# Optimization experiments

Hardware: AMD Instinct MI355X
Metric: run time of the kernel (lower is better)

Reference implementation:

```python
import jax, jax.numpy as jnp
import numpy as np

B, S, DEC, ENC = 64, 4096, 512, 256


def setup_inputs() -> dict:
    key = jax.random.key(0)
    ks = jax.random.split(key, 8)
    scale_d = 1.0 / np.sqrt(DEC)
    scale_e = 1.0 / np.sqrt(ENC)
    return {
        "decoder_hidden": jax.random.normal(ks[0], (B, 1, DEC), jnp.float32),
        "encoder_outputs": jax.random.normal(ks[1], (B, S, ENC), jnp.float32),
        "mask": jax.random.randint(ks[2], (B, S), 0, 2, jnp.int32),
        "Wd": jax.random.normal(ks[3], (DEC, ENC), jnp.float32) * scale_d,
        "bd": jnp.zeros((ENC,), jnp.float32),
        "We": jax.random.normal(ks[4], (ENC, ENC), jnp.float32) * scale_e,
        "be": jnp.zeros((ENC,), jnp.float32),
        "Wa": jax.random.normal(ks[5], (ENC,), jnp.float32) * scale_e,
        "ba": jnp.zeros((1,), jnp.float32),
    }


def reference(decoder_hidden, encoder_outputs, mask, Wd, bd, We, be, Wa, ba):
    # decoder_proj: [B,1,ENC]; encoder_proj: [B,S,ENC]
    decoder_proj = jnp.einsum("bqd,de->bqe", decoder_hidden, Wd) + bd
    encoder_proj = jnp.einsum("bse,ef->bsf", encoder_outputs, We) + be
    energy = jnp.tanh(decoder_proj + encoder_proj)          # [B,S,ENC]
    scores = jnp.einsum("bse,e->bs", energy, Wa) + ba[0]     # [B,S]
    scores = jnp.where(mask == 0, jnp.float32(-1e10), scores)
    attn = jax.nn.softmax(scores, axis=1)                    # [B,S]
    context = jnp.einsum("bs,bse->be", attn, encoder_outputs)[:, None, :]  # [B,1,ENC]
    return context, attn
```

## Files before the change

### kernel.cpp

```cpp
#include <hip/hip_runtime.h>

#define BATCH 64
#define SEQ   4096
#define DECD  512
#define ENC   256
#define TS    64
#define NCHUNK (SEQ / TS)
#define OUT_ATTN (BATCH * ENC)

typedef short  short8  __attribute__((ext_vector_type(8)));
typedef float  floatx4 __attribute__((ext_vector_type(4)));

__device__ __forceinline__ short f2bf(float f) {
    union { float f; unsigned u; } v; v.f = f;
    unsigned u = v.u;
    u += 0x7FFFu + ((u >> 16) & 1u);
    return (short)(u >> 16);
}

__device__ __forceinline__ float fast_tanh(float x) {
    x = fminf(fmaxf(x, -9.0f), 9.0f);
    float e2 = __expf(2.0f * x);
    float r  = __builtin_amdgcn_rcpf(e2 + 1.0f);
    return fmaf(-2.0f, r, 1.0f);
}

__device__ __forceinline__ void gload_lds16(const short* g, short* l) {
    __builtin_amdgcn_global_load_lds(
        (const __attribute__((address_space(1))) unsigned int*)g,
        (__attribute__((address_space(3))) unsigned int*)l,
        16, 0, 0);
}

__global__ void dp_kernel(const float* __restrict__ dh,
                          const float* __restrict__ Wd,
                          const float* __restrict__ bd,
                          const float* __restrict__ be,
                          float* __restrict__ dpb) {
    __shared__ float dhs[DECD];
    int b = blockIdx.x, t = threadIdx.x;
    dhs[t]       = dh[b * DECD + t];
    dhs[t + 256] = dh[b * DECD + t + 256];
    __syncthreads();
    float a0 = 0.f, a1 = 0.f, a2 = 0.f, a3 = 0.f;
#pragma unroll 4
    for (int d = 0; d < DECD; d += 4) {
        a0 = fmaf(dhs[d],     Wd[(d)     * ENC + t], a0);
        a1 = fmaf(dhs[d + 1], Wd[(d + 1) * ENC + t], a1);
        a2 = fmaf(dhs[d + 2], Wd[(d + 2) * ENC + t], a2);
        a3 = fmaf(dhs[d + 3], Wd[(d + 3) * ENC + t], a3);
    }
    dpb[b * ENC + t] = bd[t] + be[t] + ((a0 + a1) + (a2 + a3));
}

__global__ void pack_kernel(const float* __restrict__ We, short* __restrict__ WeF) {
    int gid  = blockIdx.x * 256 + threadIdx.x;
    int lane = gid & 63;
    int nt   = (gid >> 6) & 15;
    int kt   = gid >> 10;
    int quad = lane >> 4, l16 = lane & 15;
    int n = nt * 16 + l16;
    short8 v;
#pragma unroll
    for (int j = 0; j < 8; ++j) {
        int k = kt * 32 + quad * 8 + j;
        v[j] = f2bf(We[k * ENC + n]);
    }
    *(short8*)(WeF + gid * 8) = v;
}

__global__ __launch_bounds__(256, 4) void main_kernel(
    const float* __restrict__ enc, const int* __restrict__ mask,
    const short* __restrict__ WeF, const float* __restrict__ dpb,
    const float* __restrict__ Wa, const float* __restrict__ ba,
    float* __restrict__ out, float* __restrict__ ctx_ws, float* __restrict__ ml_ws)
{
    __shared__ short bsl[2][8192];
    __shared__ float sc[TS];
    __shared__ float dpbs[ENC];
    __shared__ float was[ENC];

    int blk   = blockIdx.x;
    int b     = blk >> 6;
    int chunk = blk & 63;
    int s_base = chunk * TS;
    int t    = threadIdx.x;
    int w    = t >> 6, lane = t & 63;
    int quad = lane >> 4, l16 = lane & 15;

    const float* encB = enc + (size_t)b * SEQ * ENC;
    int row = s_base + w * 16 + l16;
    const float* aRow = encB + (size_t)row * ENC + quad * 8;

    dpbs[t] = dpb[b * ENC + t];
    was[t]  = Wa[t];

    floatx4 acc[16];
#pragma unroll
    for (int nt = 0; nt < 16; ++nt) acc[nt] = (floatx4){0.f, 0.f, 0.f, 0.f};

#pragma unroll
    for (int j = 0; j < 4; ++j)
        gload_lds16(WeF + j * 2048 + (w * 64 + lane) * 8, &bsl[0][0] + j * 2048 + w * 512);

    floatx4 x0 = *(const floatx4*)(aRow);
    floatx4 x1 = *(const floatx4*)(aRow + 4);

    for (int kt = 0; kt < 8; ++kt) {
        __syncthreads();
        if (kt < 7) {
            const short* g = WeF + (kt + 1) * 8192;
            short* lb = &bsl[(kt + 1) & 1][0];
#pragma unroll
            for (int j = 0; j < 4; ++j)
                gload_lds16(g + j * 2048 + (w * 64 + lane) * 8, lb + j * 2048 + w * 512);
        }
        floatx4 nx0, nx1;
        if (kt < 7) {
            nx0 = *(const floatx4*)(aRow + (kt + 1) * 32);
            nx1 = *(const floatx4*)(aRow + (kt + 1) * 32 + 4);
        }
        short8 a;
#pragma unroll
        for (int j = 0; j < 4; ++j) { a[j] = f2bf(x0[j]); a[j + 4] = f2bf(x1[j]); }
        const short* bp = &bsl[kt & 1][0] + lane * 8;
#pragma unroll
        for (int nt = 0; nt < 16; ++nt) {
            short8 bf = *(const short8*)(bp + nt * 512);
            acc[nt] = __builtin_amdgcn_mfma_f32_16x16x32_bf16(a, bf, acc[nt], 0, 0, 0);
        }
        if (kt < 7) { x0 = nx0; x1 = nx1; }
    }

    float ba0 = ba[0];
    float part[4] = {0.f, 0.f, 0.f, 0.f};
#pragma unroll
    for (int nt = 0; nt < 16; ++nt) {
        int n = nt * 16 + l16;
        float wa  = was[n];
        float dpv = dpbs[n];
#pragma unroll
        for (int r = 0; r < 4; ++r)
            part[r] = fmaf(wa, fast_tanh(acc[nt][r] + dpv), part[r]);
    }
#pragma unroll
    for (int r = 0; r < 4; ++r) {
        float v = part[r];
        v += __shfl_xor(v, 1);
        v += __shfl_xor(v, 2);
        v += __shfl_xor(v, 4);
        v += __shfl_xor(v, 8);
        part[r] = v;
    }
    if (l16 == 0) {
        int idx0 = w * 16 + quad * 4;
        int s0 = s_base + idx0;
        const int4 mv = *(const int4*)(mask + b * SEQ + s0);
        int mvals[4] = {mv.x, mv.y, mv.z, mv.w};
#pragma unroll
        for (int r = 0; r < 4; ++r) {
            float scv = part[r] + ba0;
            if (mvals[r] == 0) scv = -1e10f;
            sc[idx0 + r] = scv;
            out[OUT_ATTN + (size_t)b * SEQ + s0 + r] = scv;
        }
    }
    __syncthreads();

    float v = sc[lane];
    float m = v;
    m = fmaxf(m, __shfl_xor(m, 1));
    m = fmaxf(m, __shfl_xor(m, 2));
    m = fmaxf(m, __shfl_xor(m, 4));
    m = fmaxf(m, __shfl_xor(m, 8));
    m = fmaxf(m, __shfl_xor(m, 16));
    m = fmaxf(m, __shfl_xor(m, 32));
    float e = __expf(v - m);
    float l = e;
    l += __shfl_xor(l, 1);
    l += __shfl_xor(l, 2);
    l += __shfl_xor(l, 4);
    l += __shfl_xor(l, 8);
    l += __shfl_xor(l, 16);
    l += __shfl_xor(l, 32);

    float c0 = 0.f, c1 = 0.f, c2 = 0.f, c3 = 0.f;
    const float* ep = encB + (size_t)s_base * ENC + t;
#pragma unroll 4
    for (int s2 = 0; s2 < TS; s2 += 4) {
        float w0 = __shfl(e, s2);
        float w1 = __shfl(e, s2 + 1);
        float w2 = __shfl(e, s2 + 2);
        float w3 = __shfl(e, s2 + 3);
        c0 = fmaf(w0, ep[(size_t)(s2)     * ENC], c0);
        c1 = fmaf(w1, ep[(size_t)(s2 + 1) * ENC], c1);
        c2 = fmaf(w2, ep[(size_t)(s2 + 2) * ENC], c2);
        c3 = fmaf(w3, ep[(size_t)(s2 + 3) * ENC], c3);
    }
    float ctx = (c0 + c1) + (c2 + c3);

    int cidx = b * NCHUNK + chunk;
    ctx_ws[(size_t)cidx * ENC + t] = ctx;
    if (t == 0) {
        ml_ws[cidx * 2]     = m;
        ml_ws[cidx * 2 + 1] = l;
    }
}

__global__ void final_kernel(const float* __restrict__ ctx_ws,
                             const float* __restrict__ ml_ws,
                             float* __restrict__ out) {
    int b = blockIdx.x, t = threadIdx.x;
    float m = -3.4e38f;
    for (int c = 0; c < NCHUNK; ++c)
        m = fmaxf(m, ml_ws[(b * NCHUNK + c) * 2]);
    float L = 0.f;
    for (int c = 0; c < NCHUNK; ++c)
        L += ml_ws[(b * NCHUNK + c) * 2 + 1] * __expf(ml_ws[(b * NCHUNK + c) * 2] - m);
    float inv = 1.0f / L;

    float cx = 0.f;
    for (int c = 0; c < NCHUNK; ++c)
        cx += ctx_ws[(size_t)(b * NCHUNK + c) * ENC + t] * __expf(ml_ws[(b * NCHUNK + c) * 2] - m);
    out[b * ENC + t] = cx * inv;

    for (int s = t; s < SEQ; s += 256) {
        float raw = out[OUT_ATTN + (size_t)b * SEQ + s];
        out[OUT_ATTN + (size_t)b * SEQ + s] = __expf(raw - m) * inv;
    }
}

extern "C" void kernel_launch(void* const* d_in, const int* in_sizes, int n_in,
                              void* d_out, int out_size, void* d_ws, size_t ws_size,
                              hipStream_t stream) {
    const float* dh   = (const float*)d_in[0];
    const float* enc  = (const float*)d_in[1];
    const int*   mask = (const int*)d_in[2];
    const float* Wd   = (const float*)d_in[3];
    const float* bd   = (const float*)d_in[4];
    const float* We   = (const float*)d_in[5];
    const float* be   = (const float*)d_in[6];
    const float* Wa   = (const float*)d_in[7];
    const float* ba   = (const float*)d_in[8];
    float* out = (float*)d_out;

    float* w      = (float*)d_ws;
    float* ctx_ws = w;
    float* ml_ws  = w + BATCH * NCHUNK * ENC;
    float* dpbuf  = ml_ws + BATCH * NCHUNK * 2;
    short* WeF    = (short*)(dpbuf + BATCH * ENC);

    hipLaunchKernelGGL(dp_kernel,   dim3(BATCH),           dim3(256), 0, stream, dh, Wd, bd, be, dpbuf);
    hipLaunchKernelGGL(pack_kernel, dim3(32),              dim3(256), 0, stream, We, WeF);
    hipLaunchKernelGGL(main_kernel, dim3(BATCH * NCHUNK),  dim3(256), 0, stream,
                       enc, mask, WeF, dpbuf, Wa, ba, out, ctx_ws, ml_ws);
    hipLaunchKernelGGL(final_kernel, dim3(BATCH),          dim3(256), 0, stream, ctx_ws, ml_ws, out);
}
```

Before: 444.1 us.

## Enlarge sequence tile, drop LDS B staging, split dp projection and context reduction

Raises the sequence tile from 64 to 256 rows per block with 512 threads. Each wave now computes two 16-row M tiles so every B fragment feeds two MFMAs, and B is read straight from global/L2 instead of being double-buffered through LDS with barriers. A-operand loads are prefetched three K-steps ahead. The decoder projection is split across 4 blocks per batch and summed in the main kernel, and the context partial sums are split over two thread halves with weights staged in LDS. This trades fewer blocks and more registers for less LDS traffic and fewer barriers, and leaves a redundant dpbs store that is immediately overwritten.

```diff
diff --git a/kernel.cpp b/kernel.cpp
--- a/kernel.cpp
+++ b/kernel.cpp
@@ -4,7 +4,7 @@
 #define SEQ   4096
 #define DECD  512
 #define ENC   256
-#define TS    64
+#define TS    256
 #define NCHUNK (SEQ / TS)
 #define OUT_ATTN (BATCH * ENC)
 
@@ -25,32 +25,28 @@
     return fmaf(-2.0f, r, 1.0f);
 }
 
-__device__ __forceinline__ void gload_lds16(const short* g, short* l) {
-    __builtin_amdgcn_global_load_lds(
-        (const __attribute__((address_space(1))) unsigned int*)g,
-        (__attribute__((address_space(3))) unsigned int*)l,
-        16, 0, 0);
-}
-
 __global__ void dp_kernel(const float* __restrict__ dh,
                           const float* __restrict__ Wd,
                           const float* __restrict__ bd,
                           const float* __restrict__ be,
-                          float* __restrict__ dpb) {
-    __shared__ float dhs[DECD];
-    int b = blockIdx.x, t = threadIdx.x;
-    dhs[t]       = dh[b * DECD + t];
-    dhs[t + 256] = dh[b * DECD + t + 256];
-    __syncthreads();
+                          float* __restrict__ dpb4) {
+    __shared__ float dhs[128];
+    int blk = blockIdx.x, b = blk >> 2, j = blk & 3;
+    int t = threadIdx.x;
+    if (t < 128) dhs[t] = dh[b * DECD + j * 128 + t];
+    __syncthreads();
+    const float* wp = Wd + (size_t)(j * 128) * ENC + t;
     float a0 = 0.f, a1 = 0.f, a2 = 0.f, a3 = 0.f;
 #pragma unroll 4
-    for (int d = 0; d < DECD; d += 4) {
-        a0 = fmaf(dhs[d],     Wd[(d)     * ENC + t], a0);
-        a1 = fmaf(dhs[d + 1], Wd[(d + 1) * ENC + t], a1);
-        a2 = fmaf(dhs[d + 2], Wd[(d + 2) * ENC + t], a2);
-        a3 = fmaf(dhs[d + 3], Wd[(d + 3) * ENC + t], a3);
-    }
-    dpb[b * ENC + t] = bd[t] + be[t] + ((a0 + a1) + (a2 + a3));
+    for (int d = 0; d < 128; d += 4) {
+        a0 = fmaf(dhs[d],     wp[(size_t)(d)     * ENC], a0);
+        a1 = fmaf(dhs[d + 1], wp[(size_t)(d + 1) * ENC], a1);
+        a2 = fmaf(dhs[d + 2], wp[(size_t)(d + 2) * ENC], a2);
+        a3 = fmaf(dhs[d + 3], wp[(size_t)(d + 3) * ENC], a3);
+    }
+    float r = (a0 + a1) + (a2 + a3);
+    if (j == 0) r += bd[t] + be[t];
+    dpb4[(size_t)(b * 4 + j) * ENC + t] = r;
 }
 
 __global__ void pack_kernel(const float* __restrict__ We, short* __restrict__ WeF) {
@@ -69,138 +65,164 @@
     *(short8*)(WeF + gid * 8) = v;
 }
 
-__global__ __launch_bounds__(256, 4) void main_kernel(
+__global__ __launch_bounds__(512, 2) void main_kernel(
     const float* __restrict__ enc, const int* __restrict__ mask,
-    const short* __restrict__ WeF, const float* __restrict__ dpb,
+    const short* __restrict__ WeF, const float* __restrict__ dpb4,
     const float* __restrict__ Wa, const float* __restrict__ ba,
     float* __restrict__ out, float* __restrict__ ctx_ws, float* __restrict__ ml_ws)
 {
-    __shared__ short bsl[2][8192];
     __shared__ float sc[TS];
+    __shared__ float wgt[TS];
     __shared__ float dpbs[ENC];
     __shared__ float was[ENC];
 
     int blk   = blockIdx.x;
-    int b     = blk >> 6;
-    int chunk = blk & 63;
+    int b     = blk >> 4;
+    int chunk = blk & 15;
     int s_base = chunk * TS;
     int t    = threadIdx.x;
     int w    = t >> 6, lane = t & 63;
     int quad = lane >> 4, l16 = lane & 15;
 
+    if (t < ENC) {
+        dpbs[t] = dpb4[t] + dpb4[ENC + t] + dpb4[2 * ENC + t] + dpb4[3 * ENC + t]
+                + 0.f;
+    }
+    if (t < ENC) {
+        const float* dp = dpb4 + (size_t)b * 4 * ENC;
+        dpbs[t] = dp[t] + dp[ENC + t] + dp[2 * ENC + t] + dp[3 * ENC + t];
+        was[t]  = Wa[t];
+    }
+    __syncthreads();
+
     const float* encB = enc + (size_t)b * SEQ * ENC;
-    int row = s_base + w * 16 + l16;
-    const float* aRow = encB + (size_t)row * ENC + quad * 8;
-
-    dpbs[t] = dpb[b * ENC + t];
-    was[t]  = Wa[t];
-
-    floatx4 acc[16];
-#pragma unroll
-    for (int nt = 0; nt < 16; ++nt) acc[nt] = (floatx4){0.f, 0.f, 0.f, 0.f};
-
-#pragma unroll
-    for (int j = 0; j < 4; ++j)
-        gload_lds16(WeF + j * 2048 + (w * 64 + lane) * 8, &bsl[0][0] + j * 2048 + w * 512);
-
-    floatx4 x0 = *(const floatx4*)(aRow);
-    floatx4 x1 = *(const floatx4*)(aRow + 4);
-
+    int row0 = s_base + w * 32 + l16;
+    const float* aR0 = encB + (size_t)row0 * ENC + quad * 8;
+    const float* aR1 = aR0 + 16 * ENC;
+
+    floatx4 acc[2][16];
+#pragma unroll
+    for (int mt = 0; mt < 2; ++mt)
+#pragma unroll
+        for (int nt = 0; nt < 16; ++nt)
+            acc[mt][nt] = (floatx4){0.f, 0.f, 0.f, 0.f};
+
+    floatx4 p0[3], p1[3], p2[3], p3[3];
+#pragma unroll
+    for (int p = 0; p < 3; ++p) {
+        p0[p] = *(const floatx4*)(aR0 + p * 32);
+        p1[p] = *(const floatx4*)(aR0 + p * 32 + 4);
+        p2[p] = *(const floatx4*)(aR1 + p * 32);
+        p3[p] = *(const floatx4*)(aR1 + p * 32 + 4);
+    }
+
+#pragma unroll
     for (int kt = 0; kt < 8; ++kt) {
-        __syncthreads();
-        if (kt < 7) {
-            const short* g = WeF + (kt + 1) * 8192;
-            short* lb = &bsl[(kt + 1) & 1][0];
-#pragma unroll
-            for (int j = 0; j < 4; ++j)
-                gload_lds16(g + j * 2048 + (w * 64 + lane) * 8, lb + j * 2048 + w * 512);
-        }
-        floatx4 nx0, nx1;
-        if (kt < 7) {
-            nx0 = *(const floatx4*)(aRow + (kt + 1) * 32);
-            nx1 = *(const floatx4*)(aRow + (kt + 1) * 32 + 4);
-        }
-        short8 a;
-#pragma unroll
-        for (int j = 0; j < 4; ++j) { a[j] = f2bf(x0[j]); a[j + 4] = f2bf(x1[j]); }
-        const short* bp = &bsl[kt & 1][0] + lane * 8;
-#pragma unroll
-        for (int nt = 0; nt < 16; ++nt) {
-            short8 bf = *(const short8*)(bp + nt * 512);
-            acc[nt] = __builtin_amdgcn_mfma_f32_16x16x32_bf16(a, bf, acc[nt], 0, 0, 0);
-        }
-        if (kt < 7) { x0 = nx0; x1 = nx1; }
+        const int s = kt % 3;
+        short8 a0, a1;
+#pragma unroll
+        for (int j = 0; j < 4; ++j) {
+            a0[j] = f2bf(p0[s][j]);  a0[j + 4] = f2bf(p1[s][j]);
+            a1[j] = f2bf(p2[s][j]);  a1[j + 4] = f2bf(p3[s][j]);
+        }
+        if (kt < 5) {
+            p0[s] = *(const floatx4*)(aR0 + (kt + 3) * 32);
+            p1[s] = *(const floatx4*)(aR0 + (kt + 3) * 32 + 4);
+            p2[s] = *(const floatx4*)(aR1 + (kt + 3) * 32);
+            p3[s] = *(const floatx4*)(aR1 + (kt + 3) * 32 + 4);
+        }
+        const short* bp = WeF + (size_t)(kt * 16 * 64 + lane) * 8;
+#pragma unroll
+        for (int ng = 0; ng < 4; ++ng) {
+            short8 bf0 = *(const short8*)(bp + (ng * 4 + 0) * 512);
+            short8 bf1 = *(const short8*)(bp + (ng * 4 + 1) * 512);
+            short8 bf2 = *(const short8*)(bp + (ng * 4 + 2) * 512);
+            short8 bf3 = *(const short8*)(bp + (ng * 4 + 3) * 512);
+            acc[0][ng * 4 + 0] = __builtin_amdgcn_mfma_f32_16x16x32_bf16(a0, bf0, acc[0][ng * 4 + 0], 0, 0, 0);
+            acc[1][ng * 4 + 0] = __builtin_amdgcn_mfma_f32_16x16x32_bf16(a1, bf0, acc[1][ng * 4 + 0], 0, 0, 0);
+            acc[0][ng * 4 + 1] = __builtin_amdgcn_mfma_f32_16x16x32_bf16(a0, bf1, acc[0][ng * 4 + 1], 0, 0, 0);
+            acc[1][ng * 4 + 1] = __builtin_amdgcn_mfma_f32_16x16x32_bf16(a1, bf1, acc[1][ng * 4 + 1], 0, 0, 0);
+            acc[0][ng * 4 + 2] = __builtin_amdgcn_mfma_f32_16x16x32_bf16(a0, bf2, acc[0][ng * 4 + 2], 0, 0, 0);
+            acc[1][ng * 4 + 2] = __builtin_amdgcn_mfma_f32_16x16x32_bf16(a1, bf2, acc[1][ng * 4 + 2], 0, 0, 0);
+            acc[0][ng * 4 + 3] = __builtin_amdgcn_mfma_f32_16x16x32_bf16(a0, bf3, acc[0][ng * 4 + 3], 0, 0, 0);
+            acc[1][ng * 4 + 3] = __builtin_amdgcn_mfma_f32_16x16x32_bf16(a1, bf3, acc[1][ng * 4 + 3], 0, 0, 0);
+        }
     }
 
     float ba0 = ba[0];
-    float part[4] = {0.f, 0.f, 0.f, 0.f};
+    float part[2][4] = {{0.f,0.f,0.f,0.f},{0.f,0.f,0.f,0.f}};
 #pragma unroll
     for (int nt = 0; nt < 16; ++nt) {
         int n = nt * 16 + l16;
         float wa  = was[n];
         float dpv = dpbs[n];
 #pragma unroll
-        for (int r = 0; r < 4; ++r)
-            part[r] = fmaf(wa, fast_tanh(acc[nt][r] + dpv), part[r]);
-    }
-#pragma unroll
-    for (int r = 0; r < 4; ++r) {
-        float v = part[r];
-        v += __shfl_xor(v, 1);
-        v += __shfl_xor(v, 2);
-        v += __shfl_xor(v, 4);
-        v += __shfl_xor(v, 8);
-        part[r] = v;
-    }
-    if (l16 == 0) {
-        int idx0 = w * 16 + quad * 4;
-        int s0 = s_base + idx0;
-        const int4 mv = *(const int4*)(mask + b * SEQ + s0);
-        int mvals[4] = {mv.x, mv.y, mv.z, mv.w};
+        for (int mt = 0; mt < 2; ++mt)
+#pragma unroll
+            for (int r = 0; r < 4; ++r)
+                part[mt][r] = fmaf(wa, fast_tanh(acc[mt][nt][r] + dpv), part[mt][r]);
+    }
+#pragma unroll
+    for (int mt = 0; mt < 2; ++mt) {
 #pragma unroll
         for (int r = 0; r < 4; ++r) {
-            float scv = part[r] + ba0;
-            if (mvals[r] == 0) scv = -1e10f;
-            sc[idx0 + r] = scv;
-            out[OUT_ATTN + (size_t)b * SEQ + s0 + r] = scv;
-        }
-    }
-    __syncthreads();
-
-    float v = sc[lane];
-    float m = v;
+            float v = part[mt][r];
+            v += __shfl_xor(v, 1);
+            v += __shfl_xor(v, 2);
+            v += __shfl_xor(v, 4);
+            v += __shfl_xor(v, 8);
+            part[mt][r] = v;
+        }
+        if (l16 == 0) {
+            int idx0 = w * 32 + mt * 16 + quad * 4;
+            int s0 = s_base + idx0;
+            const int4 mv = *(const int4*)(mask + b * SEQ + s0);
+            int mvals[4] = {mv.x, mv.y, mv.z, mv.w};
+#pragma unroll
+            for (int r = 0; r < 4; ++r) {
+                float scv = part[mt][r] + ba0;
+                if (mvals[r] == 0) scv = -1e10f;
+                sc[idx0 + r] = scv;
+                out[OUT_ATTN + (size_t)b * SEQ + s0 + r] = scv;
+            }
+        }
+    }
+    __syncthreads();
+
+    float v0 = sc[lane], v1 = sc[lane + 64], v2 = sc[lane + 128], v3 = sc[lane + 192];
+    float m = fmaxf(fmaxf(v0, v1), fmaxf(v2, v3));
     m = fmaxf(m, __shfl_xor(m, 1));
     m = fmaxf(m, __shfl_xor(m, 2));
     m = fmaxf(m, __shfl_xor(m, 4));
     m = fmaxf(m, __shfl_xor(m, 8));
     m = fmaxf(m, __shfl_xor(m, 16));
     m = fmaxf(m, __shfl_xor(m, 32));
-    float e = __expf(v - m);
-    float l = e;
+    float e0 = __expf(v0 - m), e1 = __expf(v1 - m), e2 = __expf(v2 - m), e3 = __expf(v3 - m);
+    float l = (e0 + e1) + (e2 + e3);
     l += __shfl_xor(l, 1);
     l += __shfl_xor(l, 2);
     l += __shfl_xor(l, 4);
     l += __shfl_xor(l, 8);
     l += __shfl_xor(l, 16);
     l += __shfl_xor(l, 32);
-
+    if (t < TS) wgt[t] = __expf(sc[t] - m);
+    __syncthreads();
+
+    int ecol = t & 255, h = t >> 8;
     float c0 = 0.f, c1 = 0.f, c2 = 0.f, c3 = 0.f;
-    const float* ep = encB + (size_t)s_base * ENC + t;
+    const float* ep = encB + (size_t)(s_base + h * 128) * ENC + ecol;
+    const float* wp = wgt + h * 128;
 #pragma unroll 4
-    for (int s2 = 0; s2 < TS; s2 += 4) {
-        float w0 = __shfl(e, s2);
-        float w1 = __shfl(e, s2 + 1);
-        float w2 = __shfl(e, s2 + 2);
-        float w3 = __shfl(e, s2 + 3);
-        c0 = fmaf(w0, ep[(size_t)(s2)     * ENC], c0);
-        c1 = fmaf(w1, ep[(size_t)(s2 + 1) * ENC], c1);
-        c2 = fmaf(w2, ep[(size_t)(s2 + 2) * ENC], c2);
-        c3 = fmaf(w3, ep[(size_t)(s2 + 3) * ENC], c3);
+    for (int s2 = 0; s2 < 128; s2 += 4) {
+        c0 = fmaf(wp[s2],     ep[(size_t)(s2)     * ENC], c0);
+        c1 = fmaf(wp[s2 + 1], ep[(size_t)(s2 + 1) * ENC], c1);
+        c2 = fmaf(wp[s2 + 2], ep[(size_t)(s2 + 2) * ENC], c2);
+        c3 = fmaf(wp[s2 + 3], ep[(size_t)(s2 + 3) * ENC], c3);
     }
     float ctx = (c0 + c1) + (c2 + c3);
 
     int cidx = b * NCHUNK + chunk;
-    ctx_ws[(size_t)cidx * ENC + t] = ctx;
+    ctx_ws[((size_t)cidx * 2 + h) * ENC + ecol] = ctx;
     if (t == 0) {
         ml_ws[cidx * 2]     = m;
         ml_ws[cidx * 2 + 1] = l;
@@ -220,8 +242,11 @@
     float inv = 1.0f / L;
 
     float cx = 0.f;
-    for (int c = 0; c < NCHUNK; ++c)
-        cx += ctx_ws[(size_t)(b * NCHUNK + c) * ENC + t] * __expf(ml_ws[(b * NCHUNK + c) * 2] - m);
+    for (int c = 0; c < NCHUNK; ++c) {
+        float sc_c = __expf(ml_ws[(b * NCHUNK + c) * 2] - m);
+        size_t base = ((size_t)(b * NCHUNK + c) * 2) * ENC + t;
+        cx += sc_c * (ctx_ws[base] + ctx_ws[base + ENC]);
+    }
     out[b * ENC + t] = cx * inv;
 
     for (int s = t; s < SEQ; s += 256) {
@@ -246,13 +271,13 @@
 
     float* w      = (float*)d_ws;
     float* ctx_ws = w;
-    float* ml_ws  = w + BATCH * NCHUNK * ENC;
-    float* dpbuf  = ml_ws + BATCH * NCHUNK * 2;
-    short* WeF    = (short*)(dpbuf + BATCH * ENC);
-
-    hipLaunchKernelGGL(dp_kernel,   dim3(BATCH),           dim3(256), 0, stream, dh, Wd, bd, be, dpbuf);
-    hipLaunchKernelGGL(pack_kernel, dim3(32),              dim3(256), 0, stream, We, WeF);
-    hipLaunchKernelGGL(main_kernel, dim3(BATCH * NCHUNK),  dim3(256), 0, stream,
-                       enc, mask, WeF, dpbuf, Wa, ba, out, ctx_ws, ml_ws);
-    hipLaunchKernelGGL(final_kernel, dim3(BATCH),          dim3(256), 0, stream, ctx_ws, ml_ws, out);
-}
+    float* ml_ws  = w + BATCH * NCHUNK * 2 * ENC;
+    float* dpb4   = ml_ws + BATCH * NCHUNK * 2;
+    short* WeF    = (short*)(dpb4 + BATCH * 4 * ENC);
+
+    hipLaunchKernelGGL(dp_kernel,   dim3(BATCH * 4),         dim3(256), 0, stream, dh, Wd, bd, be, dpb4);
+    hipLaunchKernelGGL(pack_kernel, dim3(32),                dim3(256), 0, stream, We, WeF);
+    hipLaunchKernelGGL(main_kernel, dim3(BATCH * NCHUNK),    dim3(512), 0, stream,
+                       enc, mask, WeF, dpb4, Wa, ba, out, ctx_ws, ml_ws);
+    hipLaunchKernelGGL(final_kernel, dim3(BATCH),            dim3(256), 0, stream, ctx_ws, ml_ws, out);
+}
```

After: 535.9 us. +20.7%, slower.
